# Kernel optimization log

Hardware: AMD Instinct MI355X
Metric: run time of the kernel (lower is better)

Reference implementation:

```python
import jax, jax.numpy as jnp
import numpy as np

N = 6144      # number of pedestrians
HID = 256     # hidden_dim
OUT = 32      # out_dim
NTOP = 4      # n nearest neighbours
EMB = OUT // NTOP  # per-neighbour embedding dim = 8


def setup_inputs() -> dict:
    key = jax.random.key(0)
    ks = jax.random.split(key, 12)
    r = lambda k, shp, s=1.0: (jax.random.normal(k, shp, dtype=jnp.float32) * s)
    return {
        "obs1": r(ks[0], (N, 2)),
        "obs2": r(ks[1], (N, 2)),
        "h": r(ks[2], (N, HID), 0.1),
        "c": r(ks[3], (N, HID), 0.1),
        "W_emb": r(ks[4], (4, EMB), 0.3),
        "b_emb": r(ks[5], (EMB,), 0.1),
        "W_ih": r(ks[6], (4 * HID, OUT), 0.1),
        "b_ih": r(ks[7], (4 * HID,), 0.1),
        "W_hh": r(ks[8], (4 * HID, HID), 0.1),
        "b_hh": r(ks[9], (4 * HID,), 0.1),
        "W_pool": r(ks[10], (OUT, HID), 0.1),
        "b_pool": r(ks[11], (OUT,), 0.1),
    }


def reference(obs1, obs2, h, c, W_emb, b_emb, W_ih, b_ih, W_hh, b_hh, W_pool, b_pool):
    n = obs2.shape[0]
    vel = obs2 - obs1                                   # [N,2]
    # rel_position[i, j] = obs2[j] - obs2[i]
    diff = obs2[None, :, :] - obs2[:, None, :]          # [N,N,2]
    dist = jnp.linalg.norm(diff, axis=-1)               # [N,N]
    # exclude self (torch code drops the diagonal before topk)
    dist = jnp.where(jnp.eye(n, dtype=bool), jnp.inf, dist)
    _, idx = jax.lax.top_k(-dist, NTOP)                 # [N,NTOP] indices of nearest
    nearest_pos = jnp.take_along_axis(diff, idx[:, :, None], axis=1)  # [N,NTOP,2]
    # rel_direction[i, j] = vel[j] - vel[i]
    nearest_vel = vel[idx] - vel[:, None, :]            # [N,NTOP,2]
    feat = jnp.concatenate([nearest_pos, nearest_vel], axis=-1)       # [N,NTOP,4]
    # Linear(4, EMB) + ReLU, then flatten neighbours -> [N, OUT]
    emb = jax.nn.relu(feat @ W_emb + b_emb).reshape(n, -1)
    # LSTMCell (PyTorch gate order: i, f, g, o)
    gates = emb @ W_ih.T + b_ih + h @ W_hh.T + b_hh     # [N,4*HID]
    gi, gf, gg, go = jnp.split(gates, 4, axis=-1)
    c_new = jax.nn.sigmoid(gf) * c + jax.nn.sigmoid(gi) * jnp.tanh(gg)
    h_new = jax.nn.sigmoid(go) * jnp.tanh(c_new)
    out = h_new @ W_pool.T + b_pool                     # [N,OUT]
    return out
```

## Files before the change

### kernel.cpp

```cpp
#include <hip/hip_runtime.h>
#include <math.h>

typedef unsigned short u16;
typedef unsigned long long u64;
typedef __attribute__((ext_vector_type(8))) short bf16x8;
typedef __attribute__((ext_vector_type(4))) float f32x4;

__device__ __forceinline__ float sigf(float x)  { return 1.0f / (1.0f + __expf(-x)); }
__device__ __forceinline__ float tanhf_(float x){ float e = __expf(2.0f * x); return 1.0f - 2.0f / (e + 1.0f); }
__device__ __forceinline__ u16 f2bf(float f) {
    unsigned x = __float_as_uint(f);
    return (u16)((x + 0x7fffu + ((x >> 16) & 1u)) >> 16);
}

#define INSU(KEY) do {                                                              \
    u64 _k = (KEY);                                                                 \
    k3 = (_k < k3) ? _k : k3;                                                       \
    { bool _c = k3 < k2; u64 _lo = _c ? k3 : k2, _hi = _c ? k2 : k3; k2 = _lo; k3 = _hi; } \
    { bool _c = k2 < k1; u64 _lo = _c ? k2 : k1, _hi = _c ? k1 : k2; k1 = _lo; k2 = _hi; } \
    { bool _c = k1 < k0; u64 _lo = _c ? k1 : k0, _hi = _c ? k0 : k1; k0 = _lo; k1 = _hi; } \
} while (0)

#define MRG4(X0,X1,X2,X3,Y0,Y1,Y2,Y3) do {                                          \
    float _q0 = fminf((X0),(Y3));                                                   \
    float _q1 = fminf((X1),(Y2));                                                   \
    float _q2 = fminf((X2),(Y1));                                                   \
    float _q3 = fminf((X3),(Y0));                                                   \
    float _l0 = fminf(_q0,_q2), _h0 = fmaxf(_q0,_q2);                               \
    float _l1 = fminf(_q1,_q3), _h1 = fmaxf(_q1,_q3);                               \
    (X0) = fminf(_l0,_l1); (X1) = fmaxf(_l0,_l1);                                   \
    (X2) = fminf(_h0,_h1); (X3) = fmaxf(_h0,_h1);                                   \
} while (0)

#define INS4(D, J) do {                                                              \
    float _d = (D); int _j = (J);                                                    \
    if (_d < bd3 || (_d == bd3 && _j < bj3)) {                                       \
        bd3 = _d; bj3 = _j;                                                          \
        if (bd3 < bd2 || (bd3 == bd2 && bj3 < bj2)) {                                \
            float _t = bd2; bd2 = bd3; bd3 = _t; int _u = bj2; bj2 = bj3; bj3 = _u; }\
        if (bd2 < bd1 || (bd2 == bd1 && bj2 < bj1)) {                                \
            float _t = bd1; bd1 = bd2; bd2 = _t; int _u = bj1; bj1 = bj2; bj2 = _u; }\
        if (bd1 < bd0 || (bd1 == bd0 && bj1 < bj0)) {                                \
            float _t = bd0; bd0 = bd1; bd1 = _t; int _u = bj0; bj0 = bj1; bj1 = _u; }\
    } } while (0)

__global__ void diag_kernel(float* out, int code, int out_size) {
    if (out_size > 0) out[0] = (float)code * 1.0e8f;
}

__device__ __forceinline__ void prep_item(
    int id, const float* Wih, const float* Whh, const float* Wp,
    u16* Wgf, u16* Wpf)
{
    if (id < 36864) {
        int gt = id / 576, rem = id - gt * 576;
        int kt = rem >> 6, ln = rem & 63;
        int g  = gt * 16 + (ln & 15);
        int k  = kt * 32 + (ln >> 4) * 8;
        u16* dst = Wgf + (size_t)id * 8;
        const float* src = (k < 32) ? (Wih + (size_t)g * 32 + k)
                                    : (Whh + (size_t)g * 256 + (k - 32));
        float4 v0 = ((const float4*)src)[0];
        float4 v1 = ((const float4*)src)[1];
        dst[0] = f2bf(v0.x); dst[1] = f2bf(v0.y); dst[2] = f2bf(v0.z); dst[3] = f2bf(v0.w);
        dst[4] = f2bf(v1.x); dst[5] = f2bf(v1.y); dst[6] = f2bf(v1.z); dst[7] = f2bf(v1.w);
    } else if (id < 37888) {
        int id2 = id - 36864;
        int pt = id2 >> 9, rem = id2 & 511;
        int kt = rem >> 6, ln = rem & 63;
        int o  = pt * 16 + (ln & 15);
        int k  = kt * 32 + (ln >> 4) * 8;
        u16* dst = Wpf + (size_t)id2 * 8;
        const float* src = Wp + (size_t)o * 256 + k;
        float4 v0 = ((const float4*)src)[0];
        float4 v1 = ((const float4*)src)[1];
        dst[0] = f2bf(v0.x); dst[1] = f2bf(v0.y); dst[2] = f2bf(v0.z); dst[3] = f2bf(v0.w);
        dst[4] = f2bf(v1.x); dst[5] = f2bf(v1.y); dst[6] = f2bf(v1.z); dst[7] = f2bf(v1.w);
    }
}

__global__ __launch_bounds__(512, 6) void knn_prep_lds_kernel(
    const float* __restrict__ obs1, const float* __restrict__ obs2,
    const float* __restrict__ Wemb, const float* __restrict__ bemb,
    const float* __restrict__ Wih,  const float* __restrict__ Whh,
    const float* __restrict__ Wp,
    u16* __restrict__ Wgf, u16* __restrict__ Wpf,
    int n, int knn_blocks, float* __restrict__ out)
{
    extern __shared__ __align__(16) char smem[];
    float4* s4 = (float4*)smem;
    float2* sP = (float2*)smem;

    const int t = threadIdx.x;

    if (blockIdx.x >= knn_blocks) {
        int id = (blockIdx.x - knn_blocks) * 512 + t;
        prep_item(id, Wih, Whh, Wp, Wgf, Wpf);
        return;
    }

    const float FINF = __int_as_float(0x7f800000);
    const float2* o2 = (const float2*)obs2;
    const float4* o4 = (const float4*)obs2;
    const int n2 = n >> 1;

    for (int idx = t; idx < n2; idx += 512) s4[idx] = o4[idx];
    if ((n & 1) && t == 0) sP[n - 1] = o2[n - 1];
    __syncthreads();

    const int lane = t & 63;
    const int wv   = t >> 6;
    const int i    = blockIdx.x * 8 + wv;
    if (i >= n) return;

    const float2 pi = o2[i];

    float mm0 = FINF, mm1 = FINF, mm2 = FINF, mm3 = FINF;

    int f = lane;
    for (; f + 64 < n2; f += 128) {
        float4 pa = s4[f], pb = s4[f + 64];
        int j0 = 2 * f;
        float dxa = pa.x - pi.x, dya = pa.y - pi.y;
        float da = __fadd_rn(__fmul_rn(dxa, dxa), __fmul_rn(dya, dya));
        da = (j0 == i) ? FINF : da;
        float dxb = pa.z - pi.x, dyb = pa.w - pi.y;
        float db = __fadd_rn(__fmul_rn(dxb, dxb), __fmul_rn(dyb, dyb));
        db = (j0 + 1 == i) ? FINF : db;
        mm0 = fminf(mm0, da); mm1 = fminf(mm1, db);
        int j1 = 2 * (f + 64);
        float dxc = pb.x - pi.x, dyc = pb.y - pi.y;
        float dc = __fadd_rn(__fmul_rn(dxc, dxc), __fmul_rn(dyc, dyc));
        dc = (j1 == i) ? FINF : dc;
        float dxd = pb.z - pi.x, dyd = pb.w - pi.y;
        float dd = __fadd_rn(__fmul_rn(dxd, dxd), __fmul_rn(dyd, dyd));
        dd = (j1 + 1 == i) ? FINF : dd;
        mm2 = fminf(mm2, dc); mm3 = fminf(mm3, dd);
    }
    for (; f < n2; f += 64) {
        float4 pa = s4[f];
        int j0 = 2 * f;
        float dxa = pa.x - pi.x, dya = pa.y - pi.y;
        float da = __fadd_rn(__fmul_rn(dxa, dxa), __fmul_rn(dya, dya));
        da = (j0 == i) ? FINF : da;
        float dxb = pa.z - pi.x, dyb = pa.w - pi.y;
        float db = __fadd_rn(__fmul_rn(dxb, dxb), __fmul_rn(dyb, dyb));
        db = (j0 + 1 == i) ? FINF : db;
        mm0 = fminf(mm0, da); mm1 = fminf(mm1, db);
    }
    if ((n & 1) && lane == 0) {
        float2 pj = sP[n - 1];
        float dx = pj.x - pi.x, dy = pj.y - pi.y;
        float d2 = __fadd_rn(__fmul_rn(dx, dx), __fmul_rn(dy, dy));
        d2 = (n - 1 == i) ? FINF : d2;
        mm2 = fminf(mm2, d2);
    }
    const float mn = fminf(fminf(mm0, mm1), fminf(mm2, mm3));

    float A0 = mn, A1 = FINF, A2 = FINF, A3 = FINF;
    #pragma unroll
    for (int m = 1; m < 64; m <<= 1) {
        float y0 = __shfl_xor(A0, m), y1 = __shfl_xor(A1, m);
        float y2 = __shfl_xor(A2, m), y3 = __shfl_xor(A3, m);
        MRG4(A0, A1, A2, A3, y0, y1, y2, y3);
    }
    const float thr = A3;

    u64 k0 = ~0ull, k1 = ~0ull, k2 = ~0ull, k3 = ~0ull;

    f = lane;
    for (; f < n2; f += 64) {
        float4 pa = s4[f];
        const int j0 = 2 * f;
        float dxa = pa.x - pi.x, dya = pa.y - pi.y;
        float da = __fadd_rn(__fmul_rn(dxa, dxa), __fmul_rn(dya, dya));
        if (da <= thr) {
            u64 key = (((u64)__float_as_uint(da)) << 24) | (unsigned)j0;
            key = (j0 == i) ? ~0ull : key;
            INSU(key);
        }
        float dxb = pa.z - pi.x, dyb = pa.w - pi.y;
        float db = __fadd_rn(__fmul_rn(dxb, dxb), __fmul_rn(dyb, dyb));
        if (db <= thr) {
            u64 key = (((u64)__float_as_uint(db)) << 24) | (unsigned)(j0 + 1);
            key = (j0 + 1 == i) ? ~0ull : key;
            INSU(key);
        }
    }
    if ((n & 1) && lane == 0) {
        float2 pj = sP[n - 1];
        float dx = pj.x - pi.x, dy = pj.y - pi.y;
        float d2 = __fadd_rn(__fmul_rn(dx, dx), __fmul_rn(dy, dy));
        if (d2 <= thr) {
            u64 key = (((u64)__float_as_uint(d2)) << 24) | (unsigned)(n - 1);
            key = (n - 1 == i) ? ~0ull : key;
            INSU(key);
        }
    }

    #pragma unroll
    for (int m = 1; m < 64; m <<= 1) {
        u64 o0 = __shfl_xor(k0, m), o1 = __shfl_xor(k1, m);
        u64 o2_ = __shfl_xor(k2, m), o3 = __shfl_xor(k3, m);
        INSU(o0); INSU(o1); INSU(o2_); INSU(o3);
    }

    if (lane < 4) {
        u64 kq = (lane == 0) ? k0 : (lane == 1) ? k1 : (lane == 2) ? k2 : k3;
        int jn = (int)(kq & 0xFFFFFF);
        if (jn < 0 || jn >= n) jn = 0;
        float pix = pi.x, piy = pi.y;
        float pjx = obs2[2 * jn], pjy = obs2[2 * jn + 1];
        float px = pjx - pix, py = pjy - piy;
        float vix = pix - obs1[2 * i];
        float viy = piy - obs1[2 * i + 1];
        float vx = (pjx - obs1[2 * jn])     - vix;
        float vy = (pjy - obs1[2 * jn + 1]) - viy;
        float* dst = out + (size_t)i * 32 + lane * 8;
        #pragma unroll
        for (int e = 0; e < 8; e++) {
            float a = px * Wemb[e]      + py * Wemb[8 + e]
                    + vx * Wemb[16 + e] + vy * Wemb[24 + e]
                    + bemb[e];
            dst[e] = fmaxf(a, 0.0f);
        }
    }
}

__global__ __launch_bounds__(256, 4) void knn_prep_kernel(
    const float* __restrict__ obs1, const float* __restrict__ obs2,
    const float* __restrict__ Wemb, const float* __restrict__ bemb,
    const float* __restrict__ Wih,  const float* __restrict__ Whh,
    const float* __restrict__ Wp,
    u16* __restrict__ Wgf, u16* __restrict__ Wpf,
    int n, int knn_blocks, float* __restrict__ out)
{
    const int t = threadIdx.x;

    if (blockIdx.x >= knn_blocks) {
        int id = (blockIdx.x - knn_blocks) * 256 + t;
        prep_item(id, Wih, Whh, Wp, Wgf, Wpf);
        return;
    }

    const int lane = t & 63;
    const int wv   = t >> 6;
    const int i    = blockIdx.x * 4 + wv;
    if (i >= n) return;

    const float FINF = __int_as_float(0x7f800000);
    const float2* o2 = (const float2*)obs2;
    const float4* o4 = (const float4*)obs2;
    const int n2 = n >> 1;
    const float2 pi = o2[i];

    float mm[8];
    #pragma unroll
    for (int q = 0; q < 8; q++) mm[q] = FINF;

    int f = lane;
    for (; f + 448 < n2; f += 512) {
        float4 p[8];
        #pragma unroll
        for (int q = 0; q < 8; q++) p[q] = o4[f + q * 64];
        #pragma unroll
        for (int q = 0; q < 8; q++) {
            const int j0 = 2 * (f + q * 64);
            float dxa = p[q].x - pi.x, dya = p[q].y - pi.y;
            float da = __fadd_rn(__fmul_rn(dxa, dxa), __fmul_rn(dya, dya));
            da = (j0 == i) ? FINF : da;
            float dxb = p[q].z - pi.x, dyb = p[q].w - pi.y;
            float db = __fadd_rn(__fmul_rn(dxb, dxb), __fmul_rn(dyb, dyb));
            db = (j0 + 1 == i) ? FINF : db;
            mm[q] = fminf(mm[q], fminf(da, db));
        }
    }
    for (; f < n2; f += 64) {
        float4 p = o4[f];
        const int j0 = 2 * f;
        float dxa = p.x - pi.x, dya = p.y - pi.y;
        float da = __fadd_rn(__fmul_rn(dxa, dxa), __fmul_rn(dya, dya));
        da = (j0 == i) ? FINF : da;
        float dxb = p.z - pi.x, dyb = p.w - pi.y;
        float db = __fadd_rn(__fmul_rn(dxb, dxb), __fmul_rn(dyb, dyb));
        db = (j0 + 1 == i) ? FINF : db;
        mm[0] = fminf(mm[0], fminf(da, db));
    }
    if ((n & 1) && lane == 0) {
        float2 pj = o2[n - 1];
        float dx = pj.x - pi.x, dy = pj.y - pi.y;
        float d2 = __fadd_rn(__fmul_rn(dx, dx), __fmul_rn(dy, dy));
        d2 = (n - 1 == i) ? FINF : d2;
        mm[1] = fminf(mm[1], d2);
    }
    const float mn = fminf(fminf(fminf(mm[0], mm[1]), fminf(mm[2], mm[3])),
                           fminf(fminf(mm[4], mm[5]), fminf(mm[6], mm[7])));

    float A0 = mn, A1 = FINF, A2 = FINF, A3 = FINF;
    #pragma unroll
    for (int m = 1; m < 64; m <<= 1) {
        float y0 = __shfl_xor(A0, m), y1 = __shfl_xor(A1, m);
        float y2 = __shfl_xor(A2, m), y3 = __shfl_xor(A3, m);
        MRG4(A0, A1, A2, A3, y0, y1, y2, y3);
    }
    const float thr = A3;

    u64 k0 = ~0ull, k1 = ~0ull, k2 = ~0ull, k3 = ~0ull;

    f = lane;
    for (; f < n2; f += 64) {
        float4 p = o4[f];
        const int j0 = 2 * f;
        float dxa = p.x - pi.x, dya = p.y - pi.y;
        float da = __fadd_rn(__fmul_rn(dxa, dxa), __fmul_rn(dya, dya));
        if (da <= thr) {
            u64 key = (((u64)__float_as_uint(da)) << 24) | (unsigned)j0;
            key = (j0 == i) ? ~0ull : key;
            INSU(key);
        }
        float dxb = p.z - pi.x, dyb = p.w - pi.y;
        float db = __fadd_rn(__fmul_rn(dxb, dxb), __fmul_rn(dyb, dyb));
        if (db <= thr) {
            u64 key = (((u64)__float_as_uint(db)) << 24) | (unsigned)(j0 + 1);
            key = (j0 + 1 == i) ? ~0ull : key;
            INSU(key);
        }
    }
    if ((n & 1) && lane == 0) {
        float2 pj = o2[n - 1];
        float dx = pj.x - pi.x, dy = pj.y - pi.y;
        float d2 = __fadd_rn(__fmul_rn(dx, dx), __fmul_rn(dy, dy));
        if (d2 <= thr) {
            u64 key = (((u64)__float_as_uint(d2)) << 24) | (unsigned)(n - 1);
            key = (n - 1 == i) ? ~0ull : key;
            INSU(key);
        }
    }

    #pragma unroll
    for (int m = 1; m < 64; m <<= 1) {
        u64 o0 = __shfl_xor(k0, m), o1 = __shfl_xor(k1, m);
        u64 o2_ = __shfl_xor(k2, m), o3 = __shfl_xor(k3, m);
        INSU(o0); INSU(o1); INSU(o2_); INSU(o3);
    }

    if (lane < 4) {
        u64 kq = (lane == 0) ? k0 : (lane == 1) ? k1 : (lane == 2) ? k2 : k3;
        int jn = (int)(kq & 0xFFFFFF);
        if (jn < 0 || jn >= n) jn = 0;
        float pix = pi.x, piy = pi.y;
        float pjx = obs2[2 * jn], pjy = obs2[2 * jn + 1];
        float px = pjx - pix, py = pjy - piy;
        float vix = pix - obs1[2 * i];
        float viy = piy - obs1[2 * i + 1];
        float vx = (pjx - obs1[2 * jn])     - vix;
        float vy = (pjy - obs1[2 * jn + 1]) - viy;
        float* dst = out + (size_t)i * 32 + lane * 8;
        #pragma unroll
        for (int e = 0; e < 8; e++) {
            float a = px * Wemb[e]      + py * Wemb[8 + e]
                    + vx * Wemb[16 + e] + vy * Wemb[24 + e]
                    + bemb[e];
            dst[e] = fmaxf(a, 0.0f);
        }
    }
}

__global__ __launch_bounds__(512) void lstm_kernel(
    const float* __restrict__ h,   const float* __restrict__ c,
    const u16*  __restrict__ Wgf,  const float* __restrict__ bih,
    const float* __restrict__ bhh,
    const u16*  __restrict__ Wpf,  const float* __restrict__ bp,
    int n, float* __restrict__ out)
{
    __shared__ __align__(16) char lds[35840];
    u16* sXb = (u16*)lds;
    u16* sHb = (u16*)(lds + 18944);

    const int t    = threadIdx.x;
    const int i0   = blockIdx.x * 24;
    const int lane = t & 63;
    const int wv   = t >> 6;
    const int fm   = lane & 15;
    const int fq   = lane >> 4;

    #pragma unroll
    for (int v = t; v < 32 * 32; v += 512) {
        int r = v >> 5, e = v & 31;
        int row = i0 + r;
        float val = (r < 24 && row < n) ? out[(size_t)row * 32 + e] : 0.0f;
        sXb[r * 296 + e] = f2bf(val);
    }
    #pragma unroll
    for (int f = t; f < 32 * 64; f += 512) {
        int r = f >> 6, k4 = f & 63;
        int row = i0 + r;
        float4 hv = (r < 24 && row < n) ? ((const float4*)h)[(size_t)row * 64 + k4]
                                        : make_float4(0.f, 0.f, 0.f, 0.f);
        u16* d = &sXb[r * 296 + 32 + k4 * 4];
        d[0] = f2bf(hv.x); d[1] = f2bf(hv.y); d[2] = f2bf(hv.z); d[3] = f2bf(hv.w);
    }
    __syncthreads();

    bf16x8 afr0[9], afr1[9];
    #pragma unroll
    for (int kt = 0; kt < 9; kt++) {
        afr0[kt] = *(const bf16x8*)&sXb[fm * 296 + kt * 32 + fq * 8];
        afr1[kt] = *(const bf16x8*)&sXb[(fm + 16) * 296 + kt * 32 + fq * 8];
    }

    #pragma unroll
    for (int ut2 = 0; ut2 < 2; ut2++) {
        const int ut = wv + ut2 * 8;
        const int u  = ut * 16 + fm;

        f32x4 acc0[4], acc1[4];
        #pragma unroll
        for (int jg = 0; jg < 4; jg++) { acc0[jg] = (f32x4){0.f,0.f,0.f,0.f};
                                         acc1[jg] = (f32x4){0.f,0.f,0.f,0.f}; }

        #pragma unroll
        for (int jg = 0; jg < 4; jg++) {
            const int gt = jg * 16 + ut;
            const u16* wbase = Wgf + ((size_t)gt * 9) * 512 + lane * 8;
            #pragma unroll
            for (int kt = 0; kt < 9; kt++) {
                bf16x8 bfr = *(const bf16x8*)(wbase + kt * 512);
                acc0[jg] = __builtin_amdgcn_mfma_f32_16x16x32_bf16(afr0[kt], bfr, acc0[jg], 0, 0, 0);
                acc1[jg] = __builtin_amdgcn_mfma_f32_16x16x32_bf16(afr1[kt], bfr, acc1[jg], 0, 0, 0);
            }
        }

        float b0 = bih[u]       + bhh[u];
        float b1 = bih[u + 256] + bhh[u + 256];
        float b2 = bih[u + 512] + bhh[u + 512];
        float b3 = bih[u + 768] + bhh[u + 768];

        #pragma unroll
        for (int r_ = 0; r_ < 4; r_++) {
            int rl = fq * 4 + r_;
            int row = i0 + rl;
            bool valid = (row < n);
            float cin = valid ? c[(size_t)row * 256 + u] : 0.0f;
            float gi = acc0[0][r_] + b0;
            float gf = acc0[1][r_] + b1;
            float gg = acc0[2][r_] + b2;
            float go = acc0[3][r_] + b3;
            float cn = sigf(gf) * cin + sigf(gi) * tanhf_(gg);
            float hn = sigf(go) * tanhf_(cn);
            sHb[rl * 264 + u] = valid ? f2bf(hn) : (u16)0;
        }
        #pragma unroll
        for (int r_ = 0; r_ < 4; r_++) {
            int rl = 16 + fq * 4 + r_;
            int row = i0 + rl;
            bool valid = (rl < 24) && (row < n);
            float cin = valid ? c[(size_t)row * 256 + u] : 0.0f;
            float gi = acc1[0][r_] + b0;
            float gf = acc1[1][r_] + b1;
            float gg = acc1[2][r_] + b2;
            float go = acc1[3][r_] + b3;
            float cn = sigf(gf) * cin + sigf(gi) * tanhf_(gg);
            float hn = sigf(go) * tanhf_(cn);
            sHb[rl * 264 + u] = valid ? f2bf(hn) : (u16)0;
        }
    }
    __syncthreads();

    if (wv < 4) {
        const int rt = wv >> 1;
        const int nc = wv & 1;
        bf16x8 ah[8];
        #pragma unroll
        for (int kt = 0; kt < 8; kt++)
            ah[kt] = *(const bf16x8*)&sHb[(fm + rt * 16) * 264 + kt * 32 + fq * 8];
        const u16* wbase = Wpf + ((size_t)nc * 8) * 512 + lane * 8;
        f32x4 acc = {0.f, 0.f, 0.f, 0.f};
        #pragma unroll
        for (int kt = 0; kt < 8; kt++) {
            bf16x8 bfr = *(const bf16x8*)(wbase + kt * 512);
            acc = __builtin_amdgcn_mfma_f32_16x16x32_bf16(ah[kt], bfr, acc, 0, 0, 0);
        }
        float bias = bp[nc * 16 + fm];
        #pragma unroll
        for (int r_ = 0; r_ < 4; r_++) {
            int rl = rt * 16 + fq * 4 + r_;
            int row = i0 + rl;
            if (rl < 24 && row < n) out[(size_t)row * 32 + nc * 16 + fm] = acc[r_] + bias;
        }
    }
}

__global__ __launch_bounds__(256) void nnlstm_fallback(
    const float* __restrict__ obs1, const float* __restrict__ obs2,
    const float* __restrict__ h,    const float* __restrict__ c,
    const float* __restrict__ Wemb, const float* __restrict__ bemb,
    const float* __restrict__ Wih,  const float* __restrict__ bih,
    const float* __restrict__ Whh,  const float* __restrict__ bhh,
    const float* __restrict__ Wp,   const float* __restrict__ bp,
    int n, float* __restrict__ out)
{
    __shared__ float sMd[16][64];
    __shared__ int   sMj[16][64];
    __shared__ float sX[16][292];
    __shared__ float sH[16][264];

    const int t   = threadIdx.x;
    const int sub = t & 15;
    const int ii  = t >> 4;
    const int i0  = blockIdx.x * 16;
    const int i   = i0 + ii;

    for (int v = t; v < 16 * 256; v += 256) {
        int r = v >> 8, k = v & 255;
        int row = i0 + r;
        sX[r][32 + k] = (row < n) ? h[(size_t)row * 256 + k] : 0.0f;
    }

    float bd0 = 1e30f, bd1 = 1e30f, bd2 = 1e30f, bd3 = 1e30f;
    int   bj0 = 0x7fffffff, bj1 = 0x7fffffff, bj2 = 0x7fffffff, bj3 = 0x7fffffff;

    if (i < n) {
        const float pix = obs2[2 * i];
        const float piy = obs2[2 * i + 1];
        for (int j = sub; j < n; j += 16) {
            float dx = obs2[2 * j]     - pix;
            float dy = obs2[2 * j + 1] - piy;
            float d2 = __fadd_rn(__fmul_rn(dx, dx), __fmul_rn(dy, dy));
            float dist = __fsqrt_rn(d2);
            if (j == i) continue;
            INS4(dist, j);
        }
    }
    sMd[ii][sub * 4 + 0] = bd0;  sMj[ii][sub * 4 + 0] = bj0;
    sMd[ii][sub * 4 + 1] = bd1;  sMj[ii][sub * 4 + 1] = bj1;
    sMd[ii][sub * 4 + 2] = bd2;  sMj[ii][sub * 4 + 2] = bj2;
    sMd[ii][sub * 4 + 3] = bd3;  sMj[ii][sub * 4 + 3] = bj3;
    __syncthreads();

    if (t < 16) {
        const int r = t;
        const int irow = i0 + r;
        float bd0 = 1e30f, bd1 = 1e30f, bd2 = 1e30f, bd3 = 1e30f;
        int   bj0 = 0x7fffffff, bj1 = 0x7fffffff, bj2 = 0x7fffffff, bj3 = 0x7fffffff;
        for (int q = 0; q < 64; q++) { INS4(sMd[r][q], sMj[r][q]); }

        if (irow < n) {
            float pix = obs2[2 * irow], piy = obs2[2 * irow + 1];
            float vix = pix - obs1[2 * irow];
            float viy = piy - obs1[2 * irow + 1];
            #pragma unroll
            for (int q2 = 0; q2 < 4; q2++) {
                int jn = (q2 == 0) ? bj0 : (q2 == 1) ? bj1 : (q2 == 2) ? bj2 : bj3;
                if (jn < 0 || jn >= n) jn = 0;
                float pjx = obs2[2 * jn], pjy = obs2[2 * jn + 1];
                float px = pjx - pix, py = pjy - piy;
                float vx = (pjx - obs1[2 * jn])     - vix;
                float vy = (pjy - obs1[2 * jn + 1]) - viy;
                #pragma unroll
                for (int e = 0; e < 8; e++) {
                    float a = px * Wemb[e]      + py * Wemb[8 + e]
                            + vx * Wemb[16 + e] + vy * Wemb[24 + e]
                            + bemb[e];
                    sX[r][q2 * 8 + e] = fmaxf(a, 0.0f);
                }
            }
        } else {
            for (int e = 0; e < 32; e++) sX[r][e] = 0.0f;
        }
    }
    __syncthreads();

    const int uu = t;
    float acc[4][16];
    #pragma unroll
    for (int j = 0; j < 4; j++) {
        float b = bih[uu + 256 * j] + bhh[uu + 256 * j];
        #pragma unroll
        for (int r = 0; r < 16; r++) acc[j][r] = b;
    }

    for (int kc = 0; kc < 288; kc++) {
        float w[4];
        #pragma unroll
        for (int j = 0; j < 4; j++) {
            int g = uu + 256 * j;
            w[j] = (kc < 32) ? Wih[(size_t)g * 32 + kc]
                             : Whh[(size_t)g * 256 + (kc - 32)];
        }
        #pragma unroll
        for (int r = 0; r < 16; r++) {
            float x = sX[r][kc];
            #pragma unroll
            for (int j = 0; j < 4; j++) acc[j][r] += w[j] * x;
        }
    }

    for (int r = 0; r < 16; r++) {
        int row = i0 + r;
        float cin = (row < n) ? c[(size_t)row * 256 + uu] : 0.0f;
        float cn = sigf(acc[1][r]) * cin + sigf(acc[0][r]) * tanhf(acc[2][r]);
        float hn = sigf(acc[3][r]) * tanhf(cn);
        sH[r][uu] = hn;
    }
    __syncthreads();

    for (int v = t; v < 16 * 32; v += 256) {
        int r = v >> 5, o = v & 31;
        int row = i0 + r;
        if (row >= n) continue;
        float a = bp[o];
        for (int kc = 0; kc < 256; kc++)
            a += Wp[(size_t)o * 256 + kc] * sH[r][kc];
        out[(size_t)row * 32 + o] = a;
    }
}

extern "C" void kernel_launch(void* const* d_in, const int* in_sizes, int n_in,
                              void* d_out, int out_size, void* d_ws, size_t ws_size,
                              hipStream_t stream) {
    float* out = (float*)d_out;

    int code = 0, n = 0;
    if (n_in != 12) code = 1;
    else {
        n = in_sizes[1] / 2;
        if (n <= 4 || in_sizes[1] != 2 * n)          code = 2;
        else if (in_sizes[0]  != 2 * n)              code = 3;
        else if (in_sizes[2]  != 256 * n)            code = 4;
        else if (in_sizes[3]  != 256 * n)            code = 5;
        else if (in_sizes[4]  != 32 || in_sizes[5] != 8)        code = 6;
        else if (in_sizes[6]  != 32768 || in_sizes[7] != 1024)  code = 7;
        else if (in_sizes[8]  != 262144 || in_sizes[9] != 1024) code = 8;
        else if (in_sizes[10] != 8192 || in_sizes[11] != 32)    code = 9;
        else if (out_size != 32 * n)                 code = 10;
    }
    if (code != 0) {
        diag_kernel<<<1, 1, 0, stream>>>(out, code, out_size);
        return;
    }

    const float* obs1   = (const float*)d_in[0];
    const float* obs2   = (const float*)d_in[1];
    const float* h      = (const float*)d_in[2];
    const float* c      = (const float*)d_in[3];
    const float* W_emb  = (const float*)d_in[4];
    const float* b_emb  = (const float*)d_in[5];
    const float* W_ih   = (const float*)d_in[6];
    const float* b_ih   = (const float*)d_in[7];
    const float* W_hh   = (const float*)d_in[8];
    const float* b_hh   = (const float*)d_in[9];
    const float* W_pool = (const float*)d_in[10];
    const float* b_pool = (const float*)d_in[11];

    const size_t wgf_bytes = (size_t)36864 * 8 * sizeof(u16);
    const size_t wpf_bytes = (size_t)1024 * 8 * sizeof(u16);

    if (ws_size >= wgf_bytes + wpf_bytes && n <= (1 << 24)) {
        u16* Wgf = (u16*)d_ws;
        u16* Wpf = (u16*)((char*)d_ws + wgf_bytes);
        const size_t lds_bytes = (size_t)((n + 1) & ~1) * 8;
        if (lds_bytes <= 49152) {
            int knn_blocks = (n + 7) / 8;
            int prep_blocks = (37888 + 511) / 512;
            knn_prep_lds_kernel<<<knn_blocks + prep_blocks, 512, lds_bytes, stream>>>(
                obs1, obs2, W_emb, b_emb, W_ih, W_hh, W_pool, Wgf, Wpf,
                n, knn_blocks, out);
        } else {
            int knn_blocks = (n + 3) / 4;
            knn_prep_kernel<<<knn_blocks + 148, 256, 0, stream>>>(
                obs1, obs2, W_emb, b_emb, W_ih, W_hh, W_pool, Wgf, Wpf,
                n, knn_blocks, out);
        }
        lstm_kernel<<<(n + 23) / 24, 512, 0, stream>>>(
            h, c, Wgf, b_ih, b_hh, Wpf, b_pool, n, out);
    } else {
        nnlstm_fallback<<<(n + 15) / 16, 256, 0, stream>>>(
            obs1, obs2, h, c, W_emb, b_emb, W_ih, b_ih, W_hh, b_hh,
            W_pool, b_pool, n, out);
    }
}
```

Measured before the change: 130.3 us.

## Split each KNN query across two waves in 1024-thread blocks with LDS merge

```diff
diff --git a/kernel.cpp b/kernel.cpp
--- a/kernel.cpp
+++ b/kernel.cpp
@@ -79,7 +79,7 @@
     }
 }
 
-__global__ __launch_bounds__(512, 6) void knn_prep_lds_kernel(
+__global__ __launch_bounds__(1024, 8) void knn_prep_lds_kernel(
     const float* __restrict__ obs1, const float* __restrict__ obs2,
     const float* __restrict__ Wemb, const float* __restrict__ bemb,
     const float* __restrict__ Wih,  const float* __restrict__ Whh,
@@ -88,38 +88,43 @@
     int n, int knn_blocks, float* __restrict__ out)
 {
     extern __shared__ __align__(16) char smem[];
+
+    const int t = threadIdx.x;
+
+    if (blockIdx.x >= knn_blocks) {
+        int id = (blockIdx.x - knn_blocks) * 1024 + t;
+        prep_item(id, Wih, Whh, Wp, Wgf, Wpf);
+        return;
+    }
+
     float4* s4 = (float4*)smem;
     float2* sP = (float2*)smem;
-
-    const int t = threadIdx.x;
-
-    if (blockIdx.x >= knn_blocks) {
-        int id = (blockIdx.x - knn_blocks) * 512 + t;
-        prep_item(id, Wih, Whh, Wp, Wgf, Wpf);
-        return;
-    }
+    const int n2 = n >> 1;
+    const size_t ns = (size_t)((n + 1) & ~1) * 8;
+    float* sTh = (float*)(smem + ns);
+    u64*   sKy = (u64*)(smem + ns + 256);
 
     const float FINF = __int_as_float(0x7f800000);
     const float2* o2 = (const float2*)obs2;
     const float4* o4 = (const float4*)obs2;
-    const int n2 = n >> 1;
-
-    for (int idx = t; idx < n2; idx += 512) s4[idx] = o4[idx];
+
+    for (int idx = t; idx < n2; idx += 1024) s4[idx] = o4[idx];
     if ((n & 1) && t == 0) sP[n - 1] = o2[n - 1];
     __syncthreads();
 
     const int lane = t & 63;
-    const int wv   = t >> 6;
-    const int i    = blockIdx.x * 8 + wv;
-    if (i >= n) return;
-
+    const int w    = t >> 6;
+    const int g    = w & 7;
+    const int half = w >> 3;
+    const int iraw = blockIdx.x * 8 + g;
+    const int i    = (iraw < n) ? iraw : (n - 1);
     const float2 pi = o2[i];
 
     float mm0 = FINF, mm1 = FINF, mm2 = FINF, mm3 = FINF;
 
-    int f = lane;
-    for (; f + 64 < n2; f += 128) {
-        float4 pa = s4[f], pb = s4[f + 64];
+    int f = lane + (half << 6);
+    for (; f + 128 < n2; f += 256) {
+        float4 pa = s4[f], pb = s4[f + 128];
         int j0 = 2 * f;
         float dxa = pa.x - pi.x, dya = pa.y - pi.y;
         float da = __fadd_rn(__fmul_rn(dxa, dxa), __fmul_rn(dya, dya));
@@ -128,7 +133,7 @@
         float db = __fadd_rn(__fmul_rn(dxb, dxb), __fmul_rn(dyb, dyb));
         db = (j0 + 1 == i) ? FINF : db;
         mm0 = fminf(mm0, da); mm1 = fminf(mm1, db);
-        int j1 = 2 * (f + 64);
+        int j1 = 2 * (f + 128);
         float dxc = pb.x - pi.x, dyc = pb.y - pi.y;
         float dc = __fadd_rn(__fmul_rn(dxc, dxc), __fmul_rn(dyc, dyc));
         dc = (j1 == i) ? FINF : dc;
@@ -137,7 +142,7 @@
         dd = (j1 + 1 == i) ? FINF : dd;
         mm2 = fminf(mm2, dc); mm3 = fminf(mm3, dd);
     }
-    for (; f < n2; f += 64) {
+    for (; f < n2; f += 128) {
         float4 pa = s4[f];
         int j0 = 2 * f;
         float dxa = pa.x - pi.x, dya = pa.y - pi.y;
@@ -148,7 +153,7 @@
         db = (j0 + 1 == i) ? FINF : db;
         mm0 = fminf(mm0, da); mm1 = fminf(mm1, db);
     }
-    if ((n & 1) && lane == 0) {
+    if ((n & 1) && half == 0 && lane == 0) {
         float2 pj = sP[n - 1];
         float dx = pj.x - pi.x, dy = pj.y - pi.y;
         float d2 = __fadd_rn(__fmul_rn(dx, dx), __fmul_rn(dy, dy));
@@ -164,12 +169,22 @@
         float y2 = __shfl_xor(A2, m), y3 = __shfl_xor(A3, m);
         MRG4(A0, A1, A2, A3, y0, y1, y2, y3);
     }
+    if (lane == 0) {
+        float* d = &sTh[(g * 2 + half) * 4];
+        d[0] = A0; d[1] = A1; d[2] = A2; d[3] = A3;
+    }
+    __syncthreads();
+    {
+        const float* po = &sTh[(g * 2 + (half ^ 1)) * 4];
+        float y0 = po[0], y1 = po[1], y2 = po[2], y3 = po[3];
+        MRG4(A0, A1, A2, A3, y0, y1, y2, y3);
+    }
     const float thr = A3;
 
     u64 k0 = ~0ull, k1 = ~0ull, k2 = ~0ull, k3 = ~0ull;
 
-    f = lane;
-    for (; f < n2; f += 64) {
+    f = lane + (half << 6);
+    for (; f < n2; f += 128) {
         float4 pa = s4[f];
         const int j0 = 2 * f;
         float dxa = pa.x - pi.x, dya = pa.y - pi.y;
@@ -187,7 +202,7 @@
             INSU(key);
         }
     }
-    if ((n & 1) && lane == 0) {
+    if ((n & 1) && half == 0 && lane == 0) {
         float2 pj = sP[n - 1];
         float dx = pj.x - pi.x, dy = pj.y - pi.y;
         float d2 = __fadd_rn(__fmul_rn(dx, dx), __fmul_rn(dy, dy));
@@ -204,25 +219,36 @@
         u64 o2_ = __shfl_xor(k2, m), o3 = __shfl_xor(k3, m);
         INSU(o0); INSU(o1); INSU(o2_); INSU(o3);
     }
-
-    if (lane < 4) {
-        u64 kq = (lane == 0) ? k0 : (lane == 1) ? k1 : (lane == 2) ? k2 : k3;
-        int jn = (int)(kq & 0xFFFFFF);
-        if (jn < 0 || jn >= n) jn = 0;
-        float pix = pi.x, piy = pi.y;
-        float pjx = obs2[2 * jn], pjy = obs2[2 * jn + 1];
-        float px = pjx - pix, py = pjy - piy;
-        float vix = pix - obs1[2 * i];
-        float viy = piy - obs1[2 * i + 1];
-        float vx = (pjx - obs1[2 * jn])     - vix;
-        float vy = (pjy - obs1[2 * jn + 1]) - viy;
-        float* dst = out + (size_t)i * 32 + lane * 8;
-        #pragma unroll
-        for (int e = 0; e < 8; e++) {
-            float a = px * Wemb[e]      + py * Wemb[8 + e]
-                    + vx * Wemb[16 + e] + vy * Wemb[24 + e]
-                    + bemb[e];
-            dst[e] = fmaxf(a, 0.0f);
+    if (lane == 0) {
+        u64* d = &sKy[(g * 2 + half) * 4];
+        d[0] = k0; d[1] = k1; d[2] = k2; d[3] = k3;
+    }
+    __syncthreads();
+
+    if (half == 0) {
+        const u64* pk = &sKy[(g * 2 + 1) * 4];
+        u64 p0 = pk[0], p1 = pk[1], p2 = pk[2], p3 = pk[3];
+        INSU(p0); INSU(p1); INSU(p2); INSU(p3);
+
+        if (iraw < n && lane < 4) {
+            u64 kq = (lane == 0) ? k0 : (lane == 1) ? k1 : (lane == 2) ? k2 : k3;
+            int jn = (int)(kq & 0xFFFFFF);
+            if (jn < 0 || jn >= n) jn = 0;
+            float pix = pi.x, piy = pi.y;
+            float pjx = obs2[2 * jn], pjy = obs2[2 * jn + 1];
+            float px = pjx - pix, py = pjy - piy;
+            float vix = pix - obs1[2 * i];
+            float viy = piy - obs1[2 * i + 1];
+            float vx = (pjx - obs1[2 * jn])     - vix;
+            float vy = (pjy - obs1[2 * jn + 1]) - viy;
+            float* dst = out + (size_t)i * 32 + lane * 8;
+            #pragma unroll
+            for (int e = 0; e < 8; e++) {
+                float a = px * Wemb[e]      + py * Wemb[8 + e]
+                        + vx * Wemb[16 + e] + vy * Wemb[24 + e]
+                        + bemb[e];
+                dst[e] = fmaxf(a, 0.0f);
+            }
         }
     }
 }
@@ -659,11 +685,12 @@
     if (ws_size >= wgf_bytes + wpf_bytes && n <= (1 << 24)) {
         u16* Wgf = (u16*)d_ws;
         u16* Wpf = (u16*)((char*)d_ws + wgf_bytes);
-        const size_t lds_bytes = (size_t)((n + 1) & ~1) * 8;
-        if (lds_bytes <= 49152) {
+        const size_t stage_bytes = (size_t)((n + 1) & ~1) * 8;
+        if (stage_bytes + 1024 <= 65536 && stage_bytes <= 49152) {
             int knn_blocks = (n + 7) / 8;
-            int prep_blocks = (37888 + 511) / 512;
-            knn_prep_lds_kernel<<<knn_blocks + prep_blocks, 512, lds_bytes, stream>>>(
+            int prep_blocks = (37888 + 1023) / 1024;
+            knn_prep_lds_kernel<<<knn_blocks + prep_blocks, 1024,
+                                  stage_bytes + 1024, stream>>>(
                 obs1, obs2, W_emb, b_emb, W_ih, W_hh, W_pool, Wgf, Wpf,
                 n, knn_blocks, out);
         } else {
```

Result: slower. 137.7 us (+5.6%).
